# Kernel optimization log

Hardware: AMD Instinct MI355X
Metric: run time of the kernel (lower is better)

## Reference

```python
import jax, jax.numpy as jnp
import numpy as np
from jax import lax

WIN = 9  # window side length (default [9]*ndims in the torch module)


def _box_sum3d(x, win):
    # x: [C, 1, D, H, W]; sliding-window sum with zero padding == conv3d with
    return lax.reduce_window(
        x, jnp.array(0, x.dtype), lax.add,
        window_dimensions=(1, 1, win, win, win),
        window_strides=(1, 1, 1, 1, 1),
        padding='SAME')


def setup_inputs() -> dict:
    key = jax.random.key(0)
    k1, k2 = jax.random.split(key)
    shape = (1, 2, 192, 224, 192)  # [batch, channel, D, H, W]
    y_pred = jax.random.uniform(k1, shape, dtype=jnp.float32)
    y_true = jax.random.uniform(k2, shape, dtype=jnp.float32)
    return {"y_pred": y_pred, "y_true": y_true}


def reference(y_pred, y_true):
    # permute(1, 0, 2, 3, 4): [B, C, D, H, W] -> [C, B, D, H, W]
    Ii = jnp.transpose(y_pred, (1, 0, 2, 3, 4))
    Ji = jnp.transpose(y_true, (1, 0, 2, 3, 4))
    win_size = jnp.array(WIN ** 3, Ii.dtype)

    I_sum = _box_sum3d(Ii, WIN)
    J_sum = _box_sum3d(Ji, WIN)
    I2_sum = _box_sum3d(Ii * Ii, WIN)
    J2_sum = _box_sum3d(Ji * Ji, WIN)
    IJ_sum = _box_sum3d(Ii * Ji, WIN)

    u_I = I_sum / win_size
    u_J = J_sum / win_size

    cross = IJ_sum - u_J * I_sum - u_I * J_sum + u_I * u_J * win_size
    I_var = I2_sum - 2 * u_I * I_sum + u_I * u_I * win_size
    J_var = J2_sum - 2 * u_J * J_sum + u_J * u_J * win_size

    cc = cross * cross / (I_var * J_var + 1e-5)
    return -jnp.mean(cc)
```

## Files before the change

kernel.cpp:

```cpp
#include <hip/hip_runtime.h>
#include <hip/hip_fp16.h>


#define C2   2
#define DDIM 192
#define HDIM 224
#define WDIM 192
#define HWN  (HDIM*WDIM)
#define VOL  ((size_t)DDIM*HWN)
#define RAD  4
#define WINV (1.0f/729.0f)

#define HT1  28

__device__ __forceinline__ float4 zero4() { float4 z; z.x=z.y=z.z=z.w=0.f; return z; }

__device__ __forceinline__ void padd(float4& r0, float4& r1, float4& r2,
                                     float4& r3, float4& r4,
                                     const float4 a, const float4 b) {
    r0.x+=a.x; r0.y+=a.y; r0.z+=a.z; r0.w+=a.w;
    r1.x+=b.x; r1.y+=b.y; r1.z+=b.z; r1.w+=b.w;
    r2.x=fmaf(a.x,a.x,r2.x); r2.y=fmaf(a.y,a.y,r2.y);
    r2.z=fmaf(a.z,a.z,r2.z); r2.w=fmaf(a.w,a.w,r2.w);
    r3.x=fmaf(b.x,b.x,r3.x); r3.y=fmaf(b.y,b.y,r3.y);
    r3.z=fmaf(b.z,b.z,r3.z); r3.w=fmaf(b.w,b.w,r3.w);
    r4.x=fmaf(a.x,b.x,r4.x); r4.y=fmaf(a.y,b.y,r4.y);
    r4.z=fmaf(a.z,b.z,r4.z); r4.w=fmaf(a.w,b.w,r4.w);
}
__device__ __forceinline__ void psub(float4& r0, float4& r1, float4& r2,
                                     float4& r3, float4& r4,
                                     const float4 a, const float4 b) {
    r0.x-=a.x; r0.y-=a.y; r0.z-=a.z; r0.w-=a.w;
    r1.x-=b.x; r1.y-=b.y; r1.z-=b.z; r1.w-=b.w;
    r2.x=fmaf(-a.x,a.x,r2.x); r2.y=fmaf(-a.y,a.y,r2.y);
    r2.z=fmaf(-a.z,a.z,r2.z); r2.w=fmaf(-a.w,a.w,r2.w);
    r3.x=fmaf(-b.x,b.x,r3.x); r3.y=fmaf(-b.y,b.y,r3.y);
    r3.z=fmaf(-b.z,b.z,r3.z); r3.w=fmaf(-b.w,b.w,r3.w);
    r4.x=fmaf(-a.x,b.x,r4.x); r4.y=fmaf(-a.y,b.y,r4.y);
    r4.z=fmaf(-a.z,b.z,r4.z); r4.w=fmaf(-a.w,b.w,r4.w);
}

__global__ __launch_bounds__(256)
void k_hwsum(const float* __restrict__ I, const float* __restrict__ J,
             __half* __restrict__ buf, int d0, int dbeg, int dend, int bufD)
{
    const int tid = threadIdx.x;
    const int wv  = tid >> 6;
    const int k   = tid & 63;
    const bool act = (k < 48);
    const int w0  = 4 * (act ? k : 0);
    int d = dbeg + 4*blockIdx.x + wv;
    if (d >= dend) d = dend - 1;
    const int h0 = blockIdx.y * HT1;
    const int c  = blockIdx.z;

    __shared__ float lds[4][5][208];

    if (k < 4) {
        #pragma unroll
        for (int f = 0; f < 5; ++f) lds[wv][f][4 + k] = 0.f;
    }
    if (k >= 60) {
        #pragma unroll
        for (int f = 0; f < 5; ++f) lds[wv][f][200 + (k - 60)] = 0.f;
    }

    const float* Ib = I + (size_t)c*VOL + (size_t)d*HWN + w0;
    const float* Jb = J + (size_t)c*VOL + (size_t)d*HWN + w0;

    float4 rs0=zero4(), rs1=zero4(), rs2=zero4(), rs3=zero4(), rs4=zero4();
    float4 rI0,rI1,rI2,rI3,rI4,rI5,rI6,rI7,rI8, rJ0,rJ1,rJ2,rJ3,rJ4,rJ5,rJ6,rJ7,rJ8;
    rI8 = zero4(); rJ8 = zero4();

    #define WARM(S, RIS, RJS) { const int h = h0 - RAD + S;                        \
        float4 iv = zero4(), jv = zero4();                                         \
        if (act && h >= 0 && h < HDIM) {                                           \
            iv = *(const float4*)(Ib + (size_t)h*WDIM);                            \
            jv = *(const float4*)(Jb + (size_t)h*WDIM); }                          \
        RIS = iv; RJS = jv; padd(rs0,rs1,rs2,rs3,rs4, iv, jv); }
    WARM(0,rI0,rJ0) WARM(1,rI1,rJ1) WARM(2,rI2,rJ2) WARM(3,rI3,rJ3)
    WARM(4,rI4,rJ4) WARM(5,rI5,rJ5) WARM(6,rI6,rJ6) WARM(7,rI7,rJ7)
    #undef WARM

    float4 nI = zero4(), nJ = zero4();
    if (act) {
        nI = *(const float4*)(Ib + (size_t)(h0 + RAD)*WDIM);
        nJ = *(const float4*)(Jb + (size_t)(h0 + RAD)*WDIM);
    }

    const size_t fstride = (size_t)C2*bufD*HWN;
    __half* ob = buf + ((size_t)c*bufD + (size_t)(d - d0 + RAD))*HWN + w0;

    float4* const L0 = (float4*)&lds[wv][0][0];
    float4* const L1 = (float4*)&lds[wv][1][0];
    float4* const L2 = (float4*)&lds[wv][2][0];
    float4* const L3 = (float4*)&lds[wv][3][0];
    float4* const L4 = (float4*)&lds[wv][4][0];

    int i = 0;

    #define FIELDOUT(L, RSF, F) {                                                  \
        const float4 A = L[k+1], Cc = L[k+3];                                      \
        const float o0 = ((A.x+A.y)+(A.z+A.w)) + ((RSF.x+RSF.y)+(RSF.z+RSF.w)) + Cc.x; \
        const float o1 = o0 - A.x + Cc.y;                                          \
        const float o2 = o1 - A.y + Cc.z;                                          \
        const float o3 = o2 - A.z + Cc.w;                                          \
        const __half2 ha = __floats2half2_rn(o0, o1);                              \
        const __half2 hb = __floats2half2_rn(o2, o3);                              \
        uint2 u; u.x = __builtin_bit_cast(unsigned int, ha);                       \
        u.y = __builtin_bit_cast(unsigned int, hb);                                \
        *reinterpret_cast<uint2*>(ob + (size_t)F*fstride + (size_t)h*WDIM) = u; }

    #define STEP(RID, RJD, RIS, RJS) {                                             \
        const int h = h0 + i;                                                      \
        const float4 aI = nI, aJ = nJ;                                             \
        nI = zero4(); nJ = zero4();                                                \
        { const int hf = h + 1 + RAD;                                              \
          if (act && (i + 1 < HT1) && hf < HDIM) {                                 \
              nI = *(const float4*)(Ib + (size_t)hf*WDIM);                         \
              nJ = *(const float4*)(Jb + (size_t)hf*WDIM); } }                     \
        padd(rs0,rs1,rs2,rs3,rs4, aI, aJ);                                         \
        if (act) { L0[k+2]=rs0; L1[k+2]=rs1; L2[k+2]=rs2; L3[k+2]=rs3; L4[k+2]=rs4; } \
        asm volatile("s_waitcnt lgkmcnt(0)" ::: "memory");                         \
        if (act) { FIELDOUT(L0,rs0,0) FIELDOUT(L1,rs1,1) FIELDOUT(L2,rs2,2)        \
                   FIELDOUT(L3,rs3,3) FIELDOUT(L4,rs4,4) }                         \
        psub(rs0,rs1,rs2,rs3,rs4, RID, RJD);                                       \
        RIS = aI; RJS = aJ;                                                        \
        ++i; }

    for (int s = 0; s < 3; ++s) {
        STEP(rI0,rJ0,rI8,rJ8) STEP(rI1,rJ1,rI0,rJ0) STEP(rI2,rJ2,rI1,rJ1)
        STEP(rI3,rJ3,rI2,rJ2) STEP(rI4,rJ4,rI3,rJ3) STEP(rI5,rJ5,rI4,rJ4)
        STEP(rI6,rJ6,rI5,rJ5) STEP(rI7,rJ7,rI6,rJ6) STEP(rI8,rJ8,rI7,rJ7)
    }
    STEP(rI0,rJ0,rI8,rJ8)
    #undef STEP
    #undef FIELDOUT
}

__global__ __launch_bounds__(256)
void k_dsum(const __half* __restrict__ buf, double* __restrict__ gacc,
            int d0, int bufD, int DS)
{
    const int tid = threadIdx.x;
    const int pix = blockIdx.x*256 + tid;
    const int c   = blockIdx.z;
    const int ds0 = d0 + blockIdx.y*DS;

    const size_t fstride = (size_t)C2*bufD*HWN;
    const __half* base = buf + (size_t)c*bufD*HWN + pix;

    float ring[5][9];
    float rs[5] = {0.f,0.f,0.f,0.f,0.f};
    float acc = 0.f;

    #pragma unroll
    for (int k = 0; k < 8; ++k) {
        const int dd = ds0 - RAD + k;
        float v[5] = {0.f,0.f,0.f,0.f,0.f};
        if ((unsigned)dd < (unsigned)DDIM) {
            const __half* pp = base + (size_t)(dd - d0 + RAD)*HWN;
            #pragma unroll
            for (int f = 0; f < 5; ++f) v[f] = __half2float(pp[(size_t)f*fstride]);
        }
        #pragma unroll
        for (int f = 0; f < 5; ++f) { ring[f][k] = v[f]; rs[f] += v[f]; }
    }

    int i = 0;
    while (i < DS) {
        #pragma unroll
        for (int p = 0; p < 9; ++p) {
            if (i < DS) {
                const int dd = ds0 + i + RAD;
                float v[5] = {0.f,0.f,0.f,0.f,0.f};
                if (dd < DDIM) {
                    const __half* pp = base + (size_t)(dd - d0 + RAD)*HWN;
                    #pragma unroll
                    for (int f = 0; f < 5; ++f) v[f] = __half2float(pp[(size_t)f*fstride]);
                }
                float S[5];
                #pragma unroll
                for (int f = 0; f < 5; ++f) {
                    rs[f] += v[f];
                    S[f] = rs[f];
                    rs[f] -= ring[f][p];
                    ring[f][(p+8)%9] = v[f];
                }
                const float uI    = S[0]*WINV;
                const float uJ    = S[1]*WINV;
                const float cross = S[4] - uJ*S[0];
                const float Iv    = S[2] - uI*S[0];
                const float Jv    = S[3] - uJ*S[1];
                acc += cross*cross / (Iv*Jv + 1e-5f);
                ++i;
            }
        }
    }

    __shared__ float wred[4];
    #pragma unroll
    for (int off = 32; off > 0; off >>= 1) acc += __shfl_down(acc, off);
    if ((tid & 63) == 0) wred[tid >> 6] = acc;
    __syncthreads();
    if (tid == 0) {
        const float sum = wred[0] + wred[1] + wred[2] + wred[3];
        atomicAdd(gacc, (double)sum);
    }
}

__global__ void k_fin(const double* __restrict__ gacc, float* __restrict__ out)
{
    out[0] = (float)(-gacc[0] / (double)((size_t)C2*DDIM*HDIM*WDIM));
}

extern "C" void kernel_launch(void* const* d_in, const int* in_sizes, int n_in,
                              void* d_out, int out_size, void* d_ws, size_t ws_size,
                              hipStream_t stream)
{
    if (n_in < 2) return;
    const float* I = (const float*)d_in[0];
    const float* J = (const float*)d_in[1];
    float* out = (float*)d_out;
    double* gacc = (double*)d_ws;
    __half* buf = (__half*)((char*)d_ws + 256);

    static const int cands[] = {192, 96, 48, 24, 12, 6, 4, 2, 1};
    int Dc = 0;
    for (int c : cands) {
        const size_t need = 256 + (size_t)5*C2*(c+8)*HWN*sizeof(__half);
        if (need <= ws_size) { Dc = c; break; }
    }
    if (Dc == 0) return;

    hipMemsetAsync(d_ws, 0, 256, stream);

    const int DS   = (Dc % 48 == 0) ? 48 : Dc;
    const int nsub = Dc / DS;
    const int bufD = Dc + 8;

    for (int d0 = 0; d0 < DDIM; d0 += Dc) {
        const int dbeg = (d0 - RAD < 0) ? 0 : d0 - RAD;
        const int dend = (d0 + Dc + RAD > DDIM) ? DDIM : d0 + Dc + RAD;
        const int nd   = dend - dbeg;
        dim3 g1((nd + 3)/4, HDIM/HT1, C2);
        k_hwsum<<<g1, dim3(256,1,1), 0, stream>>>(I, J, buf, d0, dbeg, dend, bufD);
        dim3 g2(HWN/256, nsub, C2);
        k_dsum<<<g2, dim3(256,1,1), 0, stream>>>(buf, gacc, d0, bufD, DS);
    }
    k_fin<<<1,1,0,stream>>>(gacc, out);
}
```

Measured before the change: 111.6 us.

## Stage fp16 box-sum rows in LDS and flush two rows as 16-byte stores

The H-pass kernel now writes each row's fp16 outputs into an LDS staging buffer and, every second row, flushes two rows per field with full 16-byte stores instead of 8-byte global stores per row. The input prefetch is deepened from one to two rows ahead, and the H tile is halved from 28 to 14 rows, which doubles the number of blocks. The goal is wider, better-coalesced global writes and more latency hiding. In exchange it adds LDS traffic, another lgkmcnt wait, extra shared memory per block, and more warm-up overhead from the 8-row halo relative to 14 output rows.

```diff
diff --git a/kernel.cpp b/kernel.cpp
--- a/kernel.cpp
+++ b/kernel.cpp
@@ -11,7 +11,7 @@
 #define RAD  4
 #define WINV (1.0f/729.0f)
 
-#define HT1  28
+#define HT1  14
 
 __device__ __forceinline__ float4 zero4() { float4 z; z.x=z.y=z.z=z.w=0.f; return z; }
 
@@ -55,6 +55,7 @@
     const int c  = blockIdx.z;
 
     __shared__ float lds[4][5][208];
+    __shared__ __align__(16) uint2 stag[4][5][96];
 
     if (k < 4) {
         #pragma unroll
@@ -82,14 +83,16 @@
     WARM(4,rI4,rJ4) WARM(5,rI5,rJ5) WARM(6,rI6,rJ6) WARM(7,rI7,rJ7)
     #undef WARM
 
-    float4 nI = zero4(), nJ = zero4();
+    float4 nI0 = zero4(), nJ0 = zero4(), nI1 = zero4(), nJ1 = zero4();
     if (act) {
-        nI = *(const float4*)(Ib + (size_t)(h0 + RAD)*WDIM);
-        nJ = *(const float4*)(Jb + (size_t)(h0 + RAD)*WDIM);
+        nI0 = *(const float4*)(Ib + (size_t)(h0 + RAD)*WDIM);
+        nJ0 = *(const float4*)(Jb + (size_t)(h0 + RAD)*WDIM);
+        nI1 = *(const float4*)(Ib + (size_t)(h0 + RAD + 1)*WDIM);
+        nJ1 = *(const float4*)(Jb + (size_t)(h0 + RAD + 1)*WDIM);
     }
 
     const size_t fstride = (size_t)C2*bufD*HWN;
-    __half* ob = buf + ((size_t)c*bufD + (size_t)(d - d0 + RAD))*HWN + w0;
+    __half* const obase = buf + ((size_t)c*bufD + (size_t)(d - d0 + RAD))*HWN;
 
     float4* const L0 = (float4*)&lds[wv][0][0];
     float4* const L1 = (float4*)&lds[wv][1][0];
@@ -99,7 +102,7 @@
 
     int i = 0;
 
-    #define FIELDOUT(L, RSF, F) {                                                  \
+    #define FIELDSTAGE(L, RSF, F, PAR) {                                           \
         const float4 A = L[k+1], Cc = L[k+3];                                      \
         const float o0 = ((A.x+A.y)+(A.z+A.w)) + ((RSF.x+RSF.y)+(RSF.z+RSF.w)) + Cc.x; \
         const float o1 = o0 - A.x + Cc.y;                                          \
@@ -109,33 +112,46 @@
         const __half2 hb = __floats2half2_rn(o2, o3);                              \
         uint2 u; u.x = __builtin_bit_cast(unsigned int, ha);                       \
         u.y = __builtin_bit_cast(unsigned int, hb);                                \
-        *reinterpret_cast<uint2*>(ob + (size_t)F*fstride + (size_t)h*WDIM) = u; }
-
-    #define STEP(RID, RJD, RIS, RJS) {                                             \
+        stag[wv][F][PAR*48 + k] = u; }
+
+    #define FLUSH(F, H) {                                                          \
+        const float4 v = ((const float4*)stag[wv][F])[k];                          \
+        *(float4*)(obase + (size_t)F*fstride + (size_t)(H)*WDIM + 8*(size_t)k) = v; }
+
+    #define STEP(PAR, RID, RJD, RIS, RJS) {                                        \
         const int h = h0 + i;                                                      \
-        const float4 aI = nI, aJ = nJ;                                             \
-        nI = zero4(); nJ = zero4();                                                \
-        { const int hf = h + 1 + RAD;                                              \
-          if (act && (i + 1 < HT1) && hf < HDIM) {                                 \
-              nI = *(const float4*)(Ib + (size_t)hf*WDIM);                         \
-              nJ = *(const float4*)(Jb + (size_t)hf*WDIM); } }                     \
+        const float4 aI = nI0, aJ = nJ0;                                           \
+        nI0 = nI1; nJ0 = nJ1;                                                      \
+        nI1 = zero4(); nJ1 = zero4();                                              \
+        { const int hf = h + 2 + RAD;                                              \
+          if (act && (i + 2 < HT1) && hf < HDIM) {                                 \
+              nI1 = *(const float4*)(Ib + (size_t)hf*WDIM);                        \
+              nJ1 = *(const float4*)(Jb + (size_t)hf*WDIM); } }                    \
         padd(rs0,rs1,rs2,rs3,rs4, aI, aJ);                                         \
         if (act) { L0[k+2]=rs0; L1[k+2]=rs1; L2[k+2]=rs2; L3[k+2]=rs3; L4[k+2]=rs4; } \
         asm volatile("s_waitcnt lgkmcnt(0)" ::: "memory");                         \
-        if (act) { FIELDOUT(L0,rs0,0) FIELDOUT(L1,rs1,1) FIELDOUT(L2,rs2,2)        \
-                   FIELDOUT(L3,rs3,3) FIELDOUT(L4,rs4,4) }                         \
+        if (act) { FIELDSTAGE(L0,rs0,0,PAR) FIELDSTAGE(L1,rs1,1,PAR)               \
+                   FIELDSTAGE(L2,rs2,2,PAR) FIELDSTAGE(L3,rs3,3,PAR)               \
+                   FIELDSTAGE(L4,rs4,4,PAR) }                                      \
+        if (PAR) {                                                                 \
+            asm volatile("s_waitcnt lgkmcnt(0)" ::: "memory");                     \
+            if (act) { FLUSH(0, h-1) FLUSH(1, h-1) FLUSH(2, h-1)                   \
+                       FLUSH(3, h-1) FLUSH(4, h-1) }                               \
+        }                                                                          \
         psub(rs0,rs1,rs2,rs3,rs4, RID, RJD);                                       \
         RIS = aI; RJS = aJ;                                                        \
         ++i; }
 
-    for (int s = 0; s < 3; ++s) {
-        STEP(rI0,rJ0,rI8,rJ8) STEP(rI1,rJ1,rI0,rJ0) STEP(rI2,rJ2,rI1,rJ1)
-        STEP(rI3,rJ3,rI2,rJ2) STEP(rI4,rJ4,rI3,rJ3) STEP(rI5,rJ5,rI4,rJ4)
-        STEP(rI6,rJ6,rI5,rJ5) STEP(rI7,rJ7,rI6,rJ6) STEP(rI8,rJ8,rI7,rJ7)
-    }
-    STEP(rI0,rJ0,rI8,rJ8)
+    STEP(0,rI0,rJ0,rI8,rJ8) STEP(1,rI1,rJ1,rI0,rJ0)
+    STEP(0,rI2,rJ2,rI1,rJ1) STEP(1,rI3,rJ3,rI2,rJ2)
+    STEP(0,rI4,rJ4,rI3,rJ3) STEP(1,rI5,rJ5,rI4,rJ4)
+    STEP(0,rI6,rJ6,rI5,rJ5) STEP(1,rI7,rJ7,rI6,rJ6)
+    STEP(0,rI8,rJ8,rI7,rJ7) STEP(1,rI0,rJ0,rI8,rJ8)
+    STEP(0,rI1,rJ1,rI0,rJ0) STEP(1,rI2,rJ2,rI1,rJ1)
+    STEP(0,rI3,rJ3,rI2,rJ2) STEP(1,rI4,rJ4,rI3,rJ3)
     #undef STEP
-    #undef FIELDOUT
+    #undef FLUSH
+    #undef FIELDSTAGE
 }
 
 __global__ __launch_bounds__(256)
```

New measurement: 116.6 us. 4.6% more time.

## Replace LDS W-halo exchange with redundant neighbor loads and 192-thread blocks

Applied to the files above, without the earlier changes.

The H/W box-sum kernel no longer shares running column sums through shared memory. Each thread now loads its left and right neighbor float4 columns and keeps three sets of running H-sums in registers. This removes the LDS stores, the lgkmcnt waits and the idle lanes of the 64-wide wavefronts (48 active of 64), packing 48 columns × 4 depth slices into 192 threads. In exchange, global/cache load traffic roughly triples and register pressure rises from carrying 15 accumulators.

```diff
diff --git a/kernel.cpp b/kernel.cpp
--- a/kernel.cpp
+++ b/kernel.cpp
@@ -40,102 +40,80 @@
     r4.z=fmaf(-a.z,b.z,r4.z); r4.w=fmaf(-a.w,b.w,r4.w);
 }
 
-__global__ __launch_bounds__(256)
+__global__ __launch_bounds__(192)
 void k_hwsum(const float* __restrict__ I, const float* __restrict__ J,
              __half* __restrict__ buf, int d0, int dbeg, int dend, int bufD)
 {
     const int tid = threadIdx.x;
-    const int wv  = tid >> 6;
-    const int k   = tid & 63;
-    const bool act = (k < 48);
-    const int w0  = 4 * (act ? k : 0);
-    int d = dbeg + 4*blockIdx.x + wv;
+    const int wg  = tid % 48;
+    const int dd  = tid / 48;
+    const int w0  = 4 * wg;
+    int d = dbeg + 4*(int)blockIdx.x + dd;
     if (d >= dend) d = dend - 1;
-    const int h0 = blockIdx.y * HT1;
-    const int c  = blockIdx.z;
-
-    __shared__ float lds[4][5][208];
-
-    if (k < 4) {
-        #pragma unroll
-        for (int f = 0; f < 5; ++f) lds[wv][f][4 + k] = 0.f;
-    }
-    if (k >= 60) {
-        #pragma unroll
-        for (int f = 0; f < 5; ++f) lds[wv][f][200 + (k - 60)] = 0.f;
-    }
-
-    const float* Ib = I + (size_t)c*VOL + (size_t)d*HWN + w0;
-    const float* Jb = J + (size_t)c*VOL + (size_t)d*HWN + w0;
-
-    float4 rs0=zero4(), rs1=zero4(), rs2=zero4(), rs3=zero4(), rs4=zero4();
-    float4 rI0,rI1,rI2,rI3,rI4,rI5,rI6,rI7,rI8, rJ0,rJ1,rJ2,rJ3,rJ4,rJ5,rJ6,rJ7,rJ8;
-    rI8 = zero4(); rJ8 = zero4();
-
-    #define WARM(S, RIS, RJS) { const int h = h0 - RAD + S;                        \
-        float4 iv = zero4(), jv = zero4();                                         \
-        if (act && h >= 0 && h < HDIM) {                                           \
-            iv = *(const float4*)(Ib + (size_t)h*WDIM);                            \
-            jv = *(const float4*)(Jb + (size_t)h*WDIM); }                          \
-        RIS = iv; RJS = jv; padd(rs0,rs1,rs2,rs3,rs4, iv, jv); }
-    WARM(0,rI0,rJ0) WARM(1,rI1,rJ1) WARM(2,rI2,rJ2) WARM(3,rI3,rJ3)
-    WARM(4,rI4,rJ4) WARM(5,rI5,rJ5) WARM(6,rI6,rJ6) WARM(7,rI7,rJ7)
-    #undef WARM
-
-    float4 nI = zero4(), nJ = zero4();
-    if (act) {
-        nI = *(const float4*)(Ib + (size_t)(h0 + RAD)*WDIM);
-        nJ = *(const float4*)(Jb + (size_t)(h0 + RAD)*WDIM);
-    }
+    const int h0 = (int)blockIdx.y * HT1;
+    const int c  = (int)blockIdx.z;
+    const bool le = (wg == 0), re = (wg == 47);
+
+    const float* __restrict__ Ib = I + (size_t)c*VOL + (size_t)d*HWN + w0;
+    const float* __restrict__ Jb = J + (size_t)c*VOL + (size_t)d*HWN + w0;
+
+    float4 L0=zero4(),L1=zero4(),L2=zero4(),L3=zero4(),L4=zero4();
+    float4 M0=zero4(),M1=zero4(),M2=zero4(),M3=zero4(),M4=zero4();
+    float4 R0=zero4(),R1=zero4(),R2=zero4(),R3=zero4(),R4=zero4();
+
+    float4 aIL,aIM,aIR,aJL,aJM,aJR;
+    float4 dIL,dIM,dIR,dJL,dJM,dJR;
+
+#define LOADROW(H, OK, IL, IM, IR, JL, JM, JR) do {                          \
+    IL = zero4(); IM = zero4(); IR = zero4();                                \
+    JL = zero4(); JM = zero4(); JR = zero4();                                \
+    if (OK) {                                                                \
+        const float* ri = Ib + (size_t)(H)*WDIM;                             \
+        const float* rj = Jb + (size_t)(H)*WDIM;                             \
+        IM = *(const float4*)ri; JM = *(const float4*)rj;                    \
+        if (!le) { IL = *(const float4*)(ri-4); JL = *(const float4*)(rj-4); } \
+        if (!re) { IR = *(const float4*)(ri+4); JR = *(const float4*)(rj+4); } \
+    } } while (0)
+
+    for (int k = 0; k < 8; ++k) {
+        const int h = h0 - RAD + k;
+        LOADROW(h, (h >= 0), dIL,dIM,dIR,dJL,dJM,dJR);
+        padd(L0,L1,L2,L3,L4, dIL, dJL);
+        padd(M0,M1,M2,M3,M4, dIM, dJM);
+        padd(R0,R1,R2,R3,R4, dIR, dJR);
+    }
+    LOADROW(h0 + RAD, true, aIL,aIM,aIR,aJL,aJM,aJR);
 
     const size_t fstride = (size_t)C2*bufD*HWN;
-    __half* ob = buf + ((size_t)c*bufD + (size_t)(d - d0 + RAD))*HWN + w0;
-
-    float4* const L0 = (float4*)&lds[wv][0][0];
-    float4* const L1 = (float4*)&lds[wv][1][0];
-    float4* const L2 = (float4*)&lds[wv][2][0];
-    float4* const L3 = (float4*)&lds[wv][3][0];
-    float4* const L4 = (float4*)&lds[wv][4][0];
-
-    int i = 0;
-
-    #define FIELDOUT(L, RSF, F) {                                                  \
-        const float4 A = L[k+1], Cc = L[k+3];                                      \
-        const float o0 = ((A.x+A.y)+(A.z+A.w)) + ((RSF.x+RSF.y)+(RSF.z+RSF.w)) + Cc.x; \
-        const float o1 = o0 - A.x + Cc.y;                                          \
-        const float o2 = o1 - A.y + Cc.z;                                          \
-        const float o3 = o2 - A.z + Cc.w;                                          \
-        const __half2 ha = __floats2half2_rn(o0, o1);                              \
-        const __half2 hb = __floats2half2_rn(o2, o3);                              \
-        uint2 u; u.x = __builtin_bit_cast(unsigned int, ha);                       \
-        u.y = __builtin_bit_cast(unsigned int, hb);                                \
-        *reinterpret_cast<uint2*>(ob + (size_t)F*fstride + (size_t)h*WDIM) = u; }
-
-    #define STEP(RID, RJD, RIS, RJS) {                                             \
-        const int h = h0 + i;                                                      \
-        const float4 aI = nI, aJ = nJ;                                             \
-        nI = zero4(); nJ = zero4();                                                \
-        { const int hf = h + 1 + RAD;                                              \
-          if (act && (i + 1 < HT1) && hf < HDIM) {                                 \
-              nI = *(const float4*)(Ib + (size_t)hf*WDIM);                         \
-              nJ = *(const float4*)(Jb + (size_t)hf*WDIM); } }                     \
-        padd(rs0,rs1,rs2,rs3,rs4, aI, aJ);                                         \
-        if (act) { L0[k+2]=rs0; L1[k+2]=rs1; L2[k+2]=rs2; L3[k+2]=rs3; L4[k+2]=rs4; } \
-        asm volatile("s_waitcnt lgkmcnt(0)" ::: "memory");                         \
-        if (act) { FIELDOUT(L0,rs0,0) FIELDOUT(L1,rs1,1) FIELDOUT(L2,rs2,2)        \
-                   FIELDOUT(L3,rs3,3) FIELDOUT(L4,rs4,4) }                         \
-        psub(rs0,rs1,rs2,rs3,rs4, RID, RJD);                                       \
-        RIS = aI; RJS = aJ;                                                        \
-        ++i; }
-
-    for (int s = 0; s < 3; ++s) {
-        STEP(rI0,rJ0,rI8,rJ8) STEP(rI1,rJ1,rI0,rJ0) STEP(rI2,rJ2,rI1,rJ1)
-        STEP(rI3,rJ3,rI2,rJ2) STEP(rI4,rJ4,rI3,rJ3) STEP(rI5,rJ5,rI4,rJ4)
-        STEP(rI6,rJ6,rI5,rJ5) STEP(rI7,rJ7,rI6,rJ6) STEP(rI8,rJ8,rI7,rJ7)
-    }
-    STEP(rI0,rJ0,rI8,rJ8)
-    #undef STEP
-    #undef FIELDOUT
+    __half* const ob = buf + ((size_t)c*bufD + (size_t)(d - d0 + RAD))*HWN + w0;
+
+#define WST(F, LL, MM, RR) {                                                 \
+    const float o0 = ((LL.x+LL.y)+(LL.z+LL.w))                               \
+                   + ((MM.x+MM.y)+(MM.z+MM.w)) + RR.x;                       \
+    const float o1 = o0 - LL.x + RR.y;                                       \
+    const float o2 = o1 - LL.y + RR.z;                                       \
+    const float o3 = o2 - LL.z + RR.w;                                       \
+    uint2 u;                                                                 \
+    u.x = __builtin_bit_cast(unsigned int, __floats2half2_rn(o0, o1));       \
+    u.y = __builtin_bit_cast(unsigned int, __floats2half2_rn(o2, o3));       \
+    *reinterpret_cast<uint2*>(ob + (size_t)(F)*fstride + (size_t)h*WDIM) = u; }
+
+    for (int i = 0; i < HT1; ++i) {
+        const int h = h0 + i;
+        LOADROW(h - RAD, (h - RAD >= 0), dIL,dIM,dIR,dJL,dJM,dJR);
+        padd(L0,L1,L2,L3,L4, aIL, aJL);
+        padd(M0,M1,M2,M3,M4, aIM, aJM);
+        padd(R0,R1,R2,R3,R4, aIR, aJR);
+        LOADROW(h + RAD + 1, (i + 1 < HT1) && (h + RAD + 1 < HDIM),
+                aIL,aIM,aIR,aJL,aJM,aJR);
+        WST(0, L0, M0, R0) WST(1, L1, M1, R1) WST(2, L2, M2, R2)
+        WST(3, L3, M3, R3) WST(4, L4, M4, R4)
+        psub(L0,L1,L2,L3,L4, dIL, dJL);
+        psub(M0,M1,M2,M3,M4, dIM, dJM);
+        psub(R0,R1,R2,R3,R4, dIR, dJR);
+    }
+#undef WST
+#undef LOADROW
 }
 
 __global__ __launch_bounds__(256)
@@ -244,7 +222,7 @@
         const int dend = (d0 + Dc + RAD > DDIM) ? DDIM : d0 + Dc + RAD;
         const int nd   = dend - dbeg;
         dim3 g1((nd + 3)/4, HDIM/HT1, C2);
-        k_hwsum<<<g1, dim3(256,1,1), 0, stream>>>(I, J, buf, d0, dbeg, dend, bufD);
+        k_hwsum<<<g1, dim3(192,1,1), 0, stream>>>(I, J, buf, d0, dbeg, dend, bufD);
         dim3 g2(HWN/256, nsub, C2);
         k_dsum<<<g2, dim3(256,1,1), 0, stream>>>(buf, gacc, d0, bufD, DS);
     }
```

After: 143.8 us. 1.29x slower.
